# Kernel optimization log

Measured on AMD Instinct MI355X. Metric: run time of the kernel, lower is better.

Reference implementation:

```python
import jax, jax.numpy as jnp
import numpy as np


def setup_inputs() -> dict:
    key = jax.random.key(0)
    k1, k2, k3, k4 = jax.random.split(key, 4)
    B, T, N, C_IN, C_OUT, K = 32, 24, 1024, 64, 64, 3
    x = jax.random.normal(k1, (B, T, N, C_IN), dtype=jnp.float32)
    Tks = jax.random.normal(k2, (K, N, N), dtype=jnp.float32)
    # kaiming-uniform-ish init scale for Theta, small uniform bias
    bound_t = float(np.sqrt(6.0 / C_IN))
    Theta = jax.random.uniform(k3, (K, C_IN, C_OUT), dtype=jnp.float32,
                               minval=-bound_t, maxval=bound_t)
    bound_b = 1.0 / float(np.sqrt(C_IN))
    bias = jax.random.uniform(k4, (K, C_OUT), dtype=jnp.float32,
                              minval=-bound_b, maxval=bound_b)
    return {"x": x, "Tks": Tks, "Theta": Theta, "bias": bias}


def reference(x, Tks, Theta, bias):
    # torch.einsum('nn,btnc->btnc', T_k, x) extracts diag(T_k) and scales x per node.
    d = jnp.diagonal(Tks, axis1=1, axis2=2)  # [K, N]
    # sum_k diag(T_k) * x @ Theta_k  -> [B, T, N, C_OUT]
    out = jnp.einsum('kn,btnc,kco->btno', d, x, Theta)
    # each bias[k] is added once -> total additive term is sum over k
    out = out + jnp.sum(bias, axis=0)
    return out
```

## Files before the change

kernel.cpp:

```cpp
#include <hip/hip_runtime.h>


#define NNODES 1024
#define CIN    64
#define COUT   64

typedef __attribute__((ext_vector_type(8))) short  short8;
typedef __attribute__((ext_vector_type(4))) float  f32x4;

__device__ __forceinline__ unsigned short f2bf(float f) {
    union { float f; unsigned u; } v; v.f = f;
    unsigned r = v.u + 0x7FFFu + ((v.u >> 16) & 1u);
    return (unsigned short)(r >> 16);
}

__global__ __launch_bounds__(256) void cheb_fused(
    const float* __restrict__ x,
    const float* __restrict__ Tks,
    const float* __restrict__ Theta,
    const float* __restrict__ bias,
    float* __restrict__ out)
{
    __shared__ __align__(16) unsigned short WT[COUT][72];
    __shared__ float bsum[COUT];

    const int blk  = blockIdx.x;
    const int n    = blk >> 1;
    const int half = blk & 1;
    const int tid  = threadIdx.x;

    const float d0 = Tks[(size_t)0 * NNODES * NNODES + (size_t)n * NNODES + n];
    const float d1 = Tks[(size_t)1 * NNODES * NNODES + (size_t)n * NNODES + n];
    const float d2 = Tks[(size_t)2 * NNODES * NNODES + (size_t)n * NNODES + n];

    for (int idx = tid; idx < CIN * COUT; idx += 256) {
        const int c = idx >> 6;
        const int o = idx & 63;
        const float w = d0 * Theta[c * 64 + o]
                      + d1 * Theta[4096 + c * 64 + o]
                      + d2 * Theta[8192 + c * 64 + o];
        WT[o][c] = f2bf(w);
    }
    if (tid < COUT) bsum[tid] = bias[tid] + bias[64 + tid] + bias[128 + tid];
    __syncthreads();

    const int wave = tid >> 6;
    const int lane = tid & 63;
    const int lrow = lane & 15;
    const int lgrp = lane >> 4;

    short8 bfrag[4][2];
    #pragma unroll
    for (int nb = 0; nb < 4; ++nb) {
        #pragma unroll
        for (int kk = 0; kk < 2; ++kk) {
            const unsigned short* p = &WT[nb * 16 + lrow][kk * 32 + lgrp * 8];
            bfrag[nb][kk] = *reinterpret_cast<const short8*>(p);
        }
    }
    float bs[4];
    #pragma unroll
    for (int nb = 0; nb < 4; ++nb) bs[nb] = bsum[nb * 16 + lrow];

    const int btbase = half * 384 + wave * 96;

    for (int it = 0; it < 6; ++it) {
        const int bt = btbase + it * 16 + lrow;
        const float* xrow = x + ((size_t)bt * NNODES + n) * CIN;
        const f32x4 xa0 = *reinterpret_cast<const f32x4*>(xrow + lgrp * 8);
        const f32x4 xa1 = *reinterpret_cast<const f32x4*>(xrow + lgrp * 8 + 4);
        const f32x4 xb0 = *reinterpret_cast<const f32x4*>(xrow + 32 + lgrp * 8);
        const f32x4 xb1 = *reinterpret_cast<const f32x4*>(xrow + 32 + lgrp * 8 + 4);

        short8 a0, a1;
        #pragma unroll
        for (int j = 0; j < 4; ++j) {
            a0[j]     = (short)f2bf(xa0[j]);
            a0[4 + j] = (short)f2bf(xa1[j]);
            a1[j]     = (short)f2bf(xb0[j]);
            a1[4 + j] = (short)f2bf(xb1[j]);
        }

        f32x4 acc[4] = {f32x4{0,0,0,0}, f32x4{0,0,0,0}, f32x4{0,0,0,0}, f32x4{0,0,0,0}};
        #pragma unroll
        for (int nb = 0; nb < 4; ++nb) {
            acc[nb] = __builtin_amdgcn_mfma_f32_16x16x32_bf16(a0, bfrag[nb][0], acc[nb], 0, 0, 0);
            acc[nb] = __builtin_amdgcn_mfma_f32_16x16x32_bf16(a1, bfrag[nb][1], acc[nb], 0, 0, 0);
        }

        const int btr = btbase + it * 16 + lgrp * 4;
        #pragma unroll
        for (int nb = 0; nb < 4; ++nb) {
            const size_t obase = ((size_t)btr * NNODES + n) * COUT + nb * 16 + lrow;
            const float bv = bs[nb];
            #pragma unroll
            for (int j = 0; j < 4; ++j) {
                out[obase + (size_t)j * NNODES * COUT] = acc[nb][j] + bv;
            }
        }
    }
}

extern "C" void kernel_launch(void* const* d_in, const int* in_sizes, int n_in,
                              void* d_out, int out_size, void* d_ws, size_t ws_size,
                              hipStream_t stream) {
    const float* x     = (const float*)d_in[0];
    const float* Tks   = (const float*)d_in[1];
    const float* Theta = (const float*)d_in[2];
    const float* bias  = (const float*)d_in[3];
    float* out = (float*)d_out;

    dim3 grid(NNODES * 2);
    dim3 block(256);
    hipLaunchKernelGGL(cheb_fused, grid, block, 0, stream, x, Tks, Theta, bias, out);
}
```

Measured before the change: 104.6 us.

## Flatten row tiling and fold diagonal scaling into activations with three MFMA passes

Blocks now cover contiguous runs of 256 flattened (b,t,n) rows instead of one node with strided batch/time rows, so x loads and output stores are contiguous. Because each row has a different node, the diagonal scaling moves from the weights onto the activations: each row is scaled by d_k before the bf16 conversion, and three separate Theta_k matrices are multiplied, which triples MFMA work and the B-fragment LDS reads. The change aims to remove the strided, poorly coalesced memory traffic of the per-node layout, at the cost of extra compute, a larger LDS footprint and a barrier in each loop iteration.

Measured after the change: 92.35 us. -11.7%, faster.

```diff
diff --git a/kernel.cpp b/kernel.cpp
--- a/kernel.cpp
+++ b/kernel.cpp
@@ -2,8 +2,9 @@
 
 
 #define NNODES 1024
-#define CIN    64
-#define COUT   64
+#define ROWS_PER_BLOCK 256
+#define NBLOCKS 3072
+#define ITERS 4
 
 typedef __attribute__((ext_vector_type(8))) short  short8;
 typedef __attribute__((ext_vector_type(4))) float  f32x4;
@@ -14,34 +15,42 @@
     return (unsigned short)(r >> 16);
 }
 
-__global__ __launch_bounds__(256) void cheb_fused(
+__global__ __launch_bounds__(256, 4) void cheb_flat(
     const float* __restrict__ x,
     const float* __restrict__ Tks,
     const float* __restrict__ Theta,
     const float* __restrict__ bias,
     float* __restrict__ out)
 {
-    __shared__ __align__(16) unsigned short WT[COUT][72];
-    __shared__ float bsum[COUT];
+    __shared__ __align__(16) unsigned short WT[3][64][72];
+    __shared__ __align__(16) float d4[ROWS_PER_BLOCK][4];
+    __shared__ float bsum[64];
 
-    const int blk  = blockIdx.x;
-    const int n    = blk >> 1;
-    const int half = blk & 1;
-    const int tid  = threadIdx.x;
+    const int tid = threadIdx.x;
+    const int rowbase = blockIdx.x * ROWS_PER_BLOCK;
 
-    const float d0 = Tks[(size_t)0 * NNODES * NNODES + (size_t)n * NNODES + n];
-    const float d1 = Tks[(size_t)1 * NNODES * NNODES + (size_t)n * NNODES + n];
-    const float d2 = Tks[(size_t)2 * NNODES * NNODES + (size_t)n * NNODES + n];
-
-    for (int idx = tid; idx < CIN * COUT; idx += 256) {
-        const int c = idx >> 6;
-        const int o = idx & 63;
-        const float w = d0 * Theta[c * 64 + o]
-                      + d1 * Theta[4096 + c * 64 + o]
-                      + d2 * Theta[8192 + c * 64 + o];
-        WT[o][c] = f2bf(w);
+    for (int idx = tid; idx < 3 * 64 * 16; idx += 256) {
+        const int k   = idx >> 10;
+        const int rem = idx & 1023;
+        const int c   = rem >> 4;
+        const int og  = (rem & 15) << 2;
+        const f32x4 th = *reinterpret_cast<const f32x4*>(Theta + k * 4096 + c * 64 + og);
+        WT[k][og + 0][c] = f2bf(th[0]);
+        WT[k][og + 1][c] = f2bf(th[1]);
+        WT[k][og + 2][c] = f2bf(th[2]);
+        WT[k][og + 3][c] = f2bf(th[3]);
     }
-    if (tid < COUT) bsum[tid] = bias[tid] + bias[64 + tid] + bias[128 + tid];
+    for (int r = tid; r < ROWS_PER_BLOCK; r += 256) {
+        const int n = (rowbase + r) & (NNODES - 1);
+        const size_t diag = (size_t)n * (NNODES + 1);
+        f32x4 v;
+        v[0] = Tks[diag];
+        v[1] = Tks[(size_t)NNODES * NNODES + diag];
+        v[2] = Tks[(size_t)2 * NNODES * NNODES + diag];
+        v[3] = 0.0f;
+        *reinterpret_cast<f32x4*>(&d4[r][0]) = v;
+    }
+    if (tid < 64) bsum[tid] = bias[tid] + bias[64 + tid] + bias[128 + tid];
     __syncthreads();
 
     const int wave = tid >> 6;
@@ -49,55 +58,60 @@
     const int lrow = lane & 15;
     const int lgrp = lane >> 4;
 
-    short8 bfrag[4][2];
-    #pragma unroll
-    for (int nb = 0; nb < 4; ++nb) {
-        #pragma unroll
-        for (int kk = 0; kk < 2; ++kk) {
-            const unsigned short* p = &WT[nb * 16 + lrow][kk * 32 + lgrp * 8];
-            bfrag[nb][kk] = *reinterpret_cast<const short8*>(p);
-        }
-    }
     float bs[4];
     #pragma unroll
     for (int nb = 0; nb < 4; ++nb) bs[nb] = bsum[nb * 16 + lrow];
 
-    const int btbase = half * 384 + wave * 96;
+    #pragma unroll 1
+    for (int it = 0; it < ITERS; ++it) {
+        const int lr  = it * 64 + wave * 16 + lrow;
+        const float* xrow = x + (size_t)(rowbase + lr) * 64;
 
-    for (int it = 0; it < 6; ++it) {
-        const int bt = btbase + it * 16 + lrow;
-        const float* xrow = x + ((size_t)bt * NNODES + n) * CIN;
-        const f32x4 xa0 = *reinterpret_cast<const f32x4*>(xrow + lgrp * 8);
-        const f32x4 xa1 = *reinterpret_cast<const f32x4*>(xrow + lgrp * 8 + 4);
-        const f32x4 xb0 = *reinterpret_cast<const f32x4*>(xrow + 32 + lgrp * 8);
-        const f32x4 xb1 = *reinterpret_cast<const f32x4*>(xrow + 32 + lgrp * 8 + 4);
+        const f32x4 x0 = *reinterpret_cast<const f32x4*>(xrow + lgrp * 8);
+        const f32x4 x1 = *reinterpret_cast<const f32x4*>(xrow + lgrp * 8 + 4);
+        const f32x4 x2 = *reinterpret_cast<const f32x4*>(xrow + 32 + lgrp * 8);
+        const f32x4 x3 = *reinterpret_cast<const f32x4*>(xrow + 32 + lgrp * 8 + 4);
 
-        short8 a0, a1;
+        const f32x4 dv = *reinterpret_cast<const f32x4*>(&d4[lr][0]);
+
+        short8 af[6];
         #pragma unroll
-        for (int j = 0; j < 4; ++j) {
-            a0[j]     = (short)f2bf(xa0[j]);
-            a0[4 + j] = (short)f2bf(xa1[j]);
-            a1[j]     = (short)f2bf(xb0[j]);
-            a1[4 + j] = (short)f2bf(xb1[j]);
+        for (int k = 0; k < 3; ++k) {
+            const float dk = dv[k];
+            #pragma unroll
+            for (int j = 0; j < 4; ++j) {
+                af[k * 2    ][j]     = (short)f2bf(dk * x0[j]);
+                af[k * 2    ][4 + j] = (short)f2bf(dk * x1[j]);
+                af[k * 2 + 1][j]     = (short)f2bf(dk * x2[j]);
+                af[k * 2 + 1][4 + j] = (short)f2bf(dk * x3[j]);
+            }
         }
 
         f32x4 acc[4] = {f32x4{0,0,0,0}, f32x4{0,0,0,0}, f32x4{0,0,0,0}, f32x4{0,0,0,0}};
         #pragma unroll
-        for (int nb = 0; nb < 4; ++nb) {
-            acc[nb] = __builtin_amdgcn_mfma_f32_16x16x32_bf16(a0, bfrag[nb][0], acc[nb], 0, 0, 0);
-            acc[nb] = __builtin_amdgcn_mfma_f32_16x16x32_bf16(a1, bfrag[nb][1], acc[nb], 0, 0, 0);
+        for (int k = 0; k < 3; ++k) {
+            #pragma unroll
+            for (int h = 0; h < 2; ++h) {
+                #pragma unroll
+                for (int nb = 0; nb < 4; ++nb) {
+                    const unsigned short* bp = &WT[k][nb * 16 + lrow][h * 32 + lgrp * 8];
+                    const short8 bf = *reinterpret_cast<const short8*>(bp);
+                    acc[nb] = __builtin_amdgcn_mfma_f32_16x16x32_bf16(af[k * 2 + h], bf, acc[nb], 0, 0, 0);
+                }
+            }
         }
 
-        const int btr = btbase + it * 16 + lgrp * 4;
+        const int orow = rowbase + it * 64 + wave * 16 + lgrp * 4;
         #pragma unroll
         for (int nb = 0; nb < 4; ++nb) {
-            const size_t obase = ((size_t)btr * NNODES + n) * COUT + nb * 16 + lrow;
             const float bv = bs[nb];
+            const size_t obase = (size_t)orow * 64 + nb * 16 + lrow;
             #pragma unroll
             for (int j = 0; j < 4; ++j) {
-                out[obase + (size_t)j * NNODES * COUT] = acc[nb][j] + bv;
+                out[obase + (size_t)j * 64] = acc[nb][j] + bv;
             }
         }
+        __syncthreads();
     }
 }
 
@@ -110,7 +124,6 @@
     const float* bias  = (const float*)d_in[3];
     float* out = (float*)d_out;
 
-    dim3 grid(NNODES * 2);
-    dim3 block(256);
-    hipLaunchKernelGGL(cheb_fused, grid, block, 0, stream, x, Tks, Theta, bias, out);
+    hipLaunchKernelGGL(cheb_flat, dim3(NBLOCKS), dim3(256), 0, stream,
+                       x, Tks, Theta, bias, out);
 }
```
